# Optimization experiments

Hardware: AMD Instinct MI355X
Metric: run time of the kernel (lower is better)

## Reference

```python
import jax, jax.numpy as jnp
import numpy as np

B, S, W, E, H, V, C = 32, 512, 15, 300, 256, 50000, 2
G = 3 * H  # stacked GRU gate dim


def setup_inputs() -> dict:
    key = jax.random.key(0)
    ks = jax.random.split(key, 20)
    f = lambda k, shape, s=0.05: jax.random.normal(k, shape, dtype=jnp.float32) * s
    return {
        "x": jax.random.randint(ks[0], (B, S), 0, V),
        "x_pre": jax.random.randint(ks[1], (B, S), 0, V),
        "x_alt": jax.random.randint(ks[2], (B, S), 0, V),
        "x_cur": jax.random.randint(ks[3], (B, S), 0, V),
        "seq_lens": jax.random.randint(ks[4], (B,), 1, S),
        "emb": f(ks[5], (V, E), 0.1),
        "W_ih_f": f(ks[6], (G, E)), "W_hh_f": f(ks[7], (G, H)),
        "b_ih_f": jnp.zeros((G,), jnp.float32), "b_hh_f": jnp.zeros((G,), jnp.float32),
        "W_ih_b": f(ks[8], (G, E)), "W_hh_b": f(ks[9], (G, H)),
        "b_ih_b": jnp.zeros((G,), jnp.float32), "b_hh_b": jnp.zeros((G,), jnp.float32),
        "bn_gamma": jnp.ones((2 * H,), jnp.float32), "bn_beta": jnp.zeros((2 * H,), jnp.float32),
        "mlp_W": f(ks[10], (2 * H, 2 * H)), "mlp_b": jnp.zeros((2 * H,), jnp.float32),
        "lin_W": f(ks[11], (C, 2 * H)), "lin_b": jnp.zeros((C,), jnp.float32),
    }


def _gru_last(xs, Wih, Whh, bih, bhh, reverse):
    """xs: [T, N, E]; returns final hidden state [N, H] of a torch-style GRU."""
    xp = jnp.einsum('tne,ge->tng', xs, Wih) + bih  # precompute input projections
    h0 = jnp.zeros((xs.shape[1], Whh.shape[1]), xs.dtype)

    def step(h, xg):
        hg = h @ Whh.T + bhh
        xr, xz, xn = jnp.split(xg, 3, axis=-1)
        hr, hz, hn = jnp.split(hg, 3, axis=-1)
        r = jax.nn.sigmoid(xr + hr)
        z = jax.nn.sigmoid(xz + hz)
        n = jnp.tanh(xn + r * hn)
        return (1.0 - z) * n + z * h, None

    h, _ = jax.lax.scan(step, h0, xp, reverse=reverse)
    return h


def reference(x, x_pre, x_alt, x_cur, seq_lens, emb,
              W_ih_f, W_hh_f, b_ih_f, b_hh_f,
              W_ih_b, W_hh_b, b_ih_b, b_hh_b,
              bn_gamma, bn_beta, mlp_W, mlp_b, lin_W, lin_b):
    mask = (x > 0).astype(jnp.float32)[:, :, None]            # [B,S,1]
    idx = jnp.arange(S)[:, None] + jnp.arange(W)[None, :]      # [S,W] window gather
    # torch pads the id tensor with 0 then embeds -> pad rows embed to emb[0]
    ef = emb[jnp.pad(x, ((0, 0), (W - 1, 0)))]                 # [B,S+W-1,E]
    et = emb[jnp.pad(x, ((0, 0), (0, W - 1)))]
    fwin = ef[:, idx].transpose(2, 0, 1, 3).reshape(W, B * S, E)
    twin = et[:, idx].transpose(2, 0, 1, 3).reshape(W, B * S, E)
    hf = _gru_last(fwin, W_ih_f, W_hh_f, b_ih_f, b_hh_f, False).reshape(B, S, H)
    hb = _gru_last(twin, W_ih_b, W_hh_b, b_ih_b, b_hh_b, True).reshape(B, S, H)
    hidden = jnp.concatenate([hf * mask, hb * mask], axis=2)   # [B,S,2H]
    # BatchNorm1d (training-mode batch stats, per channel over B and S)
    mu = hidden.mean(axis=(0, 1))
    var = ((hidden - mu) ** 2).mean(axis=(0, 1))
    normed = ((hidden - mu) / jnp.sqrt(var + 1e-5)) * bn_gamma + bn_beta
    normed = normed * mask
    mlp_h = (normed @ mlp_W.T + mlp_b) * mask + (mask - 1.0) * 65500.0
    pooled = mlp_h.max(axis=1)                                 # [B,2H] masked max-pool
    return pooled @ lin_W.T + lin_b                            # [B,C]
```

## Files before the change

### kernel.cpp

```cpp
#include <hip/hip_runtime.h>
#include <hip/hip_bf16.h>
#include <stdint.h>


typedef unsigned short u16;
typedef unsigned int u32;
typedef float f32x16 __attribute__((ext_vector_type(16)));
typedef float f32x4  __attribute__((ext_vector_type(4)));
typedef short bf16x8 __attribute__((ext_vector_type(8)));

#define MFMA32 __builtin_amdgcn_mfma_f32_32x32x16_bf16
#define MFMA16 __builtin_amdgcn_mfma_f32_16x16x32_bf16

#define NB 32
#define NS 512
#define NW 15
#define NE 300
#define NH 256
#define NG 768
#define NCELL (NB*NS)
#define EPAD 320
#define MRE 32
#define MRR 64
#define HS 264
#define WROWS 78
#define RZS 260
#define NSS 264

__device__ __forceinline__ float bf2f(u16 u){
    union { unsigned int i; float f; } v; v.i = ((unsigned int)u) << 16; return v.f;
}
__device__ __forceinline__ u16 f2bf(float f){
    union { float f; unsigned int i; } v; v.f = f;
    unsigned int x = v.i;
    x += 0x7fffu + ((x >> 16) & 1u);
    return (u16)(x >> 16);
}
__device__ __forceinline__ u16 f2bf_rh(float f){
    return (u16)((__float_as_uint(f) + 0x8000u) >> 16);
}
__device__ __forceinline__ unsigned fkey(float f){
    unsigned b = __float_as_uint(f);
    return b ^ ((b & 0x80000000u) ? 0xFFFFFFFFu : 0x80000000u);
}

__device__ __forceinline__ float sigm_hw(float x){
    return __builtin_amdgcn_rcpf(1.0f + __builtin_amdgcn_exp2f(x * -1.44269504f));
}
__device__ __forceinline__ float tanh_hw(float x){
    return fmaf(-2.0f, __builtin_amdgcn_rcpf(1.0f + __builtin_amdgcn_exp2f(x * 2.88539008f)), 1.0f);
}

__global__ void prep_kernel(const float* __restrict__ Wih_f, const float* __restrict__ Wih_b,
                            const float* __restrict__ Whh_f, const float* __restrict__ Whh_b,
                            const float* __restrict__ mlpW,
                            u16* __restrict__ WihF_p, u16* __restrict__ WihB_p,
                            u16* __restrict__ WhhF_p, u16* __restrict__ WhhB_p,
                            u16* __restrict__ mlpW_p,
                            float* __restrict__ bnSum, float* __restrict__ bnSumSq,
                            unsigned* __restrict__ pooled_u)
{
    const int tid  = blockIdx.x*blockDim.x + threadIdx.x;
    const int nthr = gridDim.x*blockDim.x;
    for (int i = tid; i < 3*8*20*64; i += nthr){
        const int lane = i & 63;
        const int t2   = i >> 6;
        const int kc   = t2 % 20;
        const int wvg  = t2 / 20;
        const int g    = wvg >> 3, wv = wvg & 7;
        const int col  = wv*32 + (lane & 31);
        const int k0   = kc*16 + (lane >> 5)*8;
        const float* sF = Wih_f + (size_t)(g*NH + col)*NE;
        const float* sB = Wih_b + (size_t)(g*NH + col)*NE;
        u16* dF = WihF_p + (size_t)i*8;
        u16* dB = WihB_p + (size_t)i*8;
        #pragma unroll
        for (int j = 0; j < 8; j++){
            const int k = k0 + j;
            dF[j] = (k < NE) ? f2bf(sF[k]) : (u16)0;
            dB[j] = (k < NE) ? f2bf(sB[k]) : (u16)0;
        }
    }
    for (int i = tid; i < 3*16*8*64; i += nthr){
        const int lane = i & 63;
        const int kc   = (i >> 6) & 7;
        const int wvg  = i >> 9;
        const int g    = wvg >> 4, wv = wvg & 15;
        const int l15  = lane & 15, q = lane >> 4;
        const int col  = wv*16 + l15;
        const int k0   = kc*32 + q*8;
        const float* srcF = Whh_f + (size_t)(g*NH + col)*NH + k0;
        const float* srcB = Whh_b + (size_t)(g*NH + col)*NH + k0;
        u16* dF = WhhF_p + (size_t)i*8;
        u16* dB = WhhB_p + (size_t)i*8;
        #pragma unroll
        for (int j = 0; j < 8; j++){ dF[j] = f2bf(srcF[j]); dB[j] = f2bf(srcB[j]); }
    }
    for (int i = tid; i < 2*8*32*64; i += nthr){
        const int lane = i & 63;
        const int t2   = i >> 6;
        const int kc   = t2 & 31;
        const int ntwv = t2 >> 5;
        const int nt   = ntwv >> 3, wv = ntwv & 7;
        const int row  = wv*64 + nt*32 + (lane & 31);
        const int k0   = kc*16 + (lane >> 5)*8;
        const float* s = mlpW + (size_t)row*512 + k0;
        u16* d = mlpW_p + (size_t)i*8;
        #pragma unroll
        for (int j = 0; j < 8; j++) d[j] = f2bf(s[j]);
    }
    for (int i = tid; i < 512; i += nthr){ bnSum[i] = 0.0f; bnSumSq[i] = 0.0f; }
    for (int i = tid; i < NB*512; i += nthr) pooled_u[i] = 0u;
}

__global__ __launch_bounds__(512, 4)
void eproj_kernel(const int* __restrict__ x, const float* __restrict__ emb,
                  const u16* __restrict__ Wih_p, const float* __restrict__ b_ih,
                  const float* __restrict__ b_hh,
                  u32* __restrict__ xprojRZ, u16* __restrict__ xprojN)
{
    __shared__ u16 a_lds[MRE*328];
    const int tid = threadIdx.x;
    const int mb  = blockIdx.x;
    {
        const int row = tid >> 4, jj = tid & 15;
        const int flat = mb*MRE + row;
        const int t_id = (flat < NCELL) ? x[flat] : 0;
        const float4* src = (const float4*)(emb + (size_t)t_id*NE);
        u16* dst = a_lds + row*328;
        for (int idx = jj; idx < 75; idx += 16){
            float4 v = src[idx];
            ushort4 o; o.x=f2bf(v.x); o.y=f2bf(v.y); o.z=f2bf(v.z); o.w=f2bf(v.w);
            *(ushort4*)(dst + idx*4) = o;
        }
        if (jj == 15){
            const ushort4 z = {0,0,0,0};
            #pragma unroll
            for (int c = 300; c < 320; c += 4) *(ushort4*)(dst + c) = z;
        }
    }
    __syncthreads();

    const int lane = tid & 63, wv = tid >> 6, l31 = lane & 31, q = lane >> 5;
    const int col = wv*32 + l31;
    f32x16 acc[3];
    #pragma unroll
    for (int g = 0; g < 3; g++)
        #pragma unroll
        for (int i = 0; i < 16; i++) acc[g][i] = 0.0f;

    const u16* a0p = a_lds + l31*328 + q*8;
    const char* wf0 = (const char*)Wih_p + (size_t)((0*8 + wv)*20)*1024 + (size_t)lane*16;
    const char* wf1 = (const char*)Wih_p + (size_t)((1*8 + wv)*20)*1024 + (size_t)lane*16;
    const char* wf2 = (const char*)Wih_p + (size_t)((2*8 + wv)*20)*1024 + (size_t)lane*16;

    #pragma unroll 4
    for (int kc = 0; kc < 20; kc++){
        bf16x8 a0 = *(const bf16x8*)(a0p + kc*16);
        bf16x8 b0 = *(const bf16x8*)(wf0 + kc*1024);
        bf16x8 b1 = *(const bf16x8*)(wf1 + kc*1024);
        bf16x8 b2 = *(const bf16x8*)(wf2 + kc*1024);
        acc[0] = MFMA32(a0,b0,acc[0],0,0,0);
        acc[1] = MFMA32(a0,b1,acc[1],0,0,0);
        acc[2] = MFMA32(a0,b2,acc[2],0,0,0);
    }
    const float br  = b_ih[col]      + b_hh[col];
    const float bz  = b_ih[NH+col]   + b_hh[NH+col];
    const float bn_ = b_ih[2*NH+col];
    #pragma unroll
    for (int r = 0; r < 16; r++){
        const int rit = (r&3) + 8*(r>>2) + 4*q;
        const int row = mb*MRE + rit;
        const u32 rzv = (u32)f2bf(acc[0][r] + br) | ((u32)f2bf(acc[1][r] + bz) << 16);
        xprojRZ[(size_t)row*256 + col] = rzv;
        xprojN [(size_t)row*256 + col] = f2bf(acc[2][r] + bn_);
    }
}

__global__ __launch_bounds__(1024, 4)
void recur_kernel(const int* __restrict__ x,
                  const u32* __restrict__ xprojRZ, const u16* __restrict__ xprojN,
                  const u16* __restrict__ Whh_p, const float* __restrict__ b_hh,
                  u16* __restrict__ hidden, float* __restrict__ bnSum, float* __restrict__ bnSumSq,
                  int dir)
{
    __shared__ u32 rz_lds[WROWS*RZS];
    __shared__ u16 n_lds [WROWS*NSS];
    __shared__ u16 h_lds [MRR*HS];
    __shared__ float maskv[MRR];
    const int tid = threadIdx.x;
    const int bid = blockIdx.x;
    const int mb  = ((bid & 7) << 5) | (bid >> 3);
    if (tid < MRR) maskv[tid] = (x[mb*MRR + tid] > 0) ? 1.0f : 0.0f;

    const int bidx = (mb*MRR) >> 9;
    const int s0   = (mb*MRR) & (NS-1);
    const int joff = s0 + (dir ? 0 : -(NW-1));

    for (int i = tid; i < WROWS*64; i += 1024){
        const int w = i >> 6, c4 = i & 63;
        const int j = joff + w;
        const size_t row = ((unsigned)j < (unsigned)NS) ? (size_t)(bidx*NS + j) : (size_t)NCELL;
        const uint4 v = *(const uint4*)(xprojRZ + row*256 + c4*4);
        *(uint4*)(rz_lds + w*RZS + c4*4) = v;
    }
    for (int i = tid; i < WROWS*32; i += 1024){
        const int w = i >> 5, c8 = i & 31;
        const int j = joff + w;
        const size_t row = ((unsigned)j < (unsigned)NS) ? (size_t)(bidx*NS + j) : (size_t)NCELL;
        const uint4 v = *(const uint4*)(xprojN + row*256 + c8*8);
        *(uint4*)(n_lds + w*NSS + c8*8) = v;
    }
    __syncthreads();

    const int lane = tid & 63, wv = tid >> 6;
    const int l15 = lane & 15, q = lane >> 4;
    const int col  = wv*16 + l15;

    const float bhn = b_hh[2*NH + col];

    const char* wf = (const char*)Whh_p + ((size_t)wv << 13) + ((size_t)lane << 4);

    const int haOff = l15*HS + q*8;
    const u32* rzp0 = rz_lds + q*4*RZS + col;
    const u16* nnp0 = n_lds  + q*4*NSS + col;

    float hreg[16];
    #pragma unroll
    for (int i = 0; i < 16; i++) hreg[i] = 0.0f;

    #pragma unroll 1
    for (int t = 0; t < NW; t++){
        f32x4 acc[4][3];
        #pragma unroll
        for (int mt = 0; mt < 4; mt++)
            #pragma unroll
            for (int g = 0; g < 3; g++)
                #pragma unroll
                for (int i = 0; i < 4; i++) acc[mt][g][i] = (g == 2) ? bhn : 0.0f;

        if (t > 0){
            const u16* hcur = h_lds + haOff;
            bf16x8 b0 = *(const bf16x8*)(wf + 0*131072);
            bf16x8 b1 = *(const bf16x8*)(wf + 1*131072);
            bf16x8 b2 = *(const bf16x8*)(wf + 2*131072);
            #pragma unroll
            for (int kc = 0; kc < 8; kc++){
                bf16x8 n0, n1, n2;
                if (kc < 7){
                    const int ko = (kc+1)*1024;
                    n0 = *(const bf16x8*)(wf + 0*131072 + ko);
                    n1 = *(const bf16x8*)(wf + 1*131072 + ko);
                    n2 = *(const bf16x8*)(wf + 2*131072 + ko);
                }
                bf16x8 a0 = *(const bf16x8*)(hcur + kc*32 +   0);
                bf16x8 a1 = *(const bf16x8*)(hcur + kc*32 + 16*HS);
                bf16x8 a2 = *(const bf16x8*)(hcur + kc*32 + 32*HS);
                bf16x8 a3 = *(const bf16x8*)(hcur + kc*32 + 48*HS);
                acc[0][0] = MFMA16(a0,b0,acc[0][0],0,0,0);
                acc[1][0] = MFMA16(a1,b0,acc[1][0],0,0,0);
                acc[2][0] = MFMA16(a2,b0,acc[2][0],0,0,0);
                acc[3][0] = MFMA16(a3,b0,acc[3][0],0,0,0);
                acc[0][1] = MFMA16(a0,b1,acc[0][1],0,0,0);
                acc[1][1] = MFMA16(a1,b1,acc[1][1],0,0,0);
                acc[2][1] = MFMA16(a2,b1,acc[2][1],0,0,0);
                acc[3][1] = MFMA16(a3,b1,acc[3][1],0,0,0);
                acc[0][2] = MFMA16(a0,b2,acc[0][2],0,0,0);
                acc[1][2] = MFMA16(a1,b2,acc[1][2],0,0,0);
                acc[2][2] = MFMA16(a2,b2,acc[2][2],0,0,0);
                acc[3][2] = MFMA16(a3,b2,acc[3][2],0,0,0);
                if (kc < 7){ b0 = n0; b1 = n1; b2 = n2; }
            }
        }
        const int wbase = (dir == 0) ? t : ((NW-1) - t);
        const u32* rzp = rzp0 + wbase*RZS;
        const u16* nnp = nnp0 + wbase*NSS;
        #pragma unroll
        for (int half = 0; half < 2; half++){
            u32 rz[8]; u16 nn[8];
            #pragma unroll
            for (int i = 0; i < 8; i++){
                const int ii = half*8 + i;
                const int mt = ii >> 2, r = ii & 3;
                rz[i] = rzp[(mt*16 + r)*RZS];
                nn[i] = nnp[(mt*16 + r)*NSS];
            }
            #pragma unroll
            for (int i = 0; i < 8; i++){
                const int ii = half*8 + i;
                const int mt = ii >> 2, r = ii & 3;
                const float xr = bf2f((u16)(rz[i] & 0xFFFFu));
                const float xz = bf2f((u16)(rz[i] >> 16));
                const float xn = bf2f(nn[i]);
                const float rg = sigm_hw(xr + acc[mt][0][r]);
                const float zg = sigm_hw(xz + acc[mt][1][r]);
                const float ng = tanh_hw(fmaf(rg, acc[mt][2][r], xn));
                hreg[ii] = fmaf(zg, hreg[ii] - ng, ng);
            }
        }
        if (t + 1 < NW){
            __syncthreads();
            #pragma unroll
            for (int mt = 0; mt < 4; mt++)
                #pragma unroll
                for (int r = 0; r < 4; r++){
                    const int rit = mt*16 + q*4 + r;
                    h_lds[rit*HS + col] = f2bf_rh(hreg[mt*4 + r]);
                }
            __syncthreads();
        }
    }
    float sum = 0.0f, sumsq = 0.0f;
    #pragma unroll
    for (int mt = 0; mt < 4; mt++)
        #pragma unroll
        for (int r = 0; r < 4; r++){
            const int rit = mt*16 + q*4 + r;
            const float hm = hreg[mt*4 + r] * maskv[rit];
            hidden[(size_t)(mb*MRR + rit)*512 + dir*NH + col] = f2bf(hm);
            sum += hm; sumsq += hm*hm;
        }
    sum   += __shfl_xor(sum, 16);   sumsq += __shfl_xor(sumsq, 16);
    sum   += __shfl_xor(sum, 32);   sumsq += __shfl_xor(sumsq, 32);
    if (q == 0){
        atomicAdd(&bnSum[dir*NH + col], sum);
        atomicAdd(&bnSumSq[dir*NH + col], sumsq);
    }
}

__global__ void bnfin_kernel(const float* __restrict__ bnSum, const float* __restrict__ bnSumSq,
                             const float* __restrict__ gamma, const float* __restrict__ beta,
                             float* __restrict__ bnScale, float* __restrict__ bnShift)
{
    const int c = blockIdx.x*blockDim.x + threadIdx.x;
    if (c < 512){
        const float mu  = bnSum[c]   * (1.0f/16384.0f);
        const float var = bnSumSq[c] * (1.0f/16384.0f) - mu*mu;
        const float inv = rsqrtf(var + 1e-5f);
        const float sc  = gamma[c]*inv;
        bnScale[c] = sc;
        bnShift[c] = beta[c] - mu*sc;
    }
}

__global__ __launch_bounds__(512, 4)
void mlp_kernel(const int* __restrict__ x, const u16* __restrict__ hidden,
                const u16* __restrict__ mlpW_p, const float* __restrict__ bnScale,
                const float* __restrict__ bnShift, const float* __restrict__ mlp_b,
                unsigned* __restrict__ pooled_u)
{
    __shared__ u16 a_lds[MRE*520];
    __shared__ float maskv[MRE];
    const int tid = threadIdx.x;
    const int mb  = blockIdx.x;
    if (tid < MRE) maskv[tid] = (x[mb*MRE + tid] > 0) ? 1.0f : 0.0f;
    __syncthreads();
    {
        const int row = tid >> 4, jj = tid & 15;
        const float m = maskv[row];
        const u16* src = hidden + (size_t)(mb*MRE + row)*512;
        u16* dst = a_lds + row*520;
        for (int c4 = jj; c4 < 128; c4 += 16){
            ushort4 v = ((const ushort4*)src)[c4];
            const int c = c4*4;
            float4 sc = *(const float4*)(bnScale + c);
            float4 sh = *(const float4*)(bnShift + c);
            ushort4 o;
            o.x = f2bf((bf2f(v.x)*sc.x + sh.x)*m);
            o.y = f2bf((bf2f(v.y)*sc.y + sh.y)*m);
            o.z = f2bf((bf2f(v.z)*sc.z + sh.z)*m);
            o.w = f2bf((bf2f(v.w)*sc.w + sh.w)*m);
            *(ushort4*)(dst + c) = o;
        }
    }
    __syncthreads();

    const int lane = tid & 63, wv = tid >> 6, l31 = lane & 31, q = lane >> 5;
    f32x16 acc[2];
    #pragma unroll
    for (int g = 0; g < 2; g++)
        #pragma unroll
        for (int i = 0; i < 16; i++) acc[g][i] = 0.0f;

    const u16* a0p = a_lds + l31*520 + q*8;
    const char* wm0 = (const char*)mlpW_p + (size_t)((0*8 + wv)*32)*1024 + (size_t)lane*16;
    const char* wm1 = (const char*)mlpW_p + (size_t)((1*8 + wv)*32)*1024 + (size_t)lane*16;

    #pragma unroll 4
    for (int kc = 0; kc < 32; kc++){
        bf16x8 a0 = *(const bf16x8*)(a0p + kc*16);
        bf16x8 b0 = *(const bf16x8*)(wm0 + kc*1024);
        bf16x8 b1 = *(const bf16x8*)(wm1 + kc*1024);
        acc[0] = MFMA32(a0,b0,acc[0],0,0,0);
        acc[1] = MFMA32(a0,b1,acc[1],0,0,0);
    }

    const int bidx = mb >> 4;
    #pragma unroll
    for (int nt = 0; nt < 2; nt++){
        const int colg = wv*64 + nt*32 + l31;
        const float bias = mlp_b[colg];
        float mx = -3.4e38f;
        #pragma unroll
        for (int r = 0; r < 16; r++){
            const int rit = (r&3) + 8*(r>>2) + 4*q;
            const float m = maskv[rit];
            const float v = (acc[nt][r] + bias)*m + (m - 1.0f)*65500.0f;
            mx = fmaxf(mx, v);
        }
        mx = fmaxf(mx, __shfl_xor(mx, 32));
        if (q == 0) atomicMax(&pooled_u[bidx*512 + colg], fkey(mx));
    }
}

__global__ void final_kernel(const unsigned* __restrict__ pooled_u,
                             const float* __restrict__ linW, const float* __restrict__ linb,
                             float* __restrict__ out)
{
    const int b = blockIdx.x;
    const int lane = threadIdx.x;
    float s0 = 0.0f, s1 = 0.0f;
    for (int c = lane; c < 512; c += 64){
        const unsigned u = pooled_u[b*512 + c];
        const unsigned bits = (u & 0x80000000u) ? (u ^ 0x80000000u) : ~u;
        const float f = __uint_as_float(bits);
        s0 += f * linW[c];
        s1 += f * linW[512 + c];
    }
    #pragma unroll
    for (int off = 32; off > 0; off >>= 1){
        s0 += __shfl_xor(s0, off);
        s1 += __shfl_xor(s1, off);
    }
    if (lane == 0){ out[2*b] = s0 + linb[0]; out[2*b + 1] = s1 + linb[1]; }
}

extern "C" void kernel_launch(void* const* d_in, const int* in_sizes, int n_in,
                              void* d_out, int out_size, void* d_ws, size_t ws_size,
                              hipStream_t stream)
{
    const int*   x     = (const int*)  d_in[0];
    const float* emb   = (const float*)d_in[5];
    const float* Wih_f = (const float*)d_in[6];
    const float* Whh_f = (const float*)d_in[7];
    const float* bih_f = (const float*)d_in[8];
    const float* bhh_f = (const float*)d_in[9];
    const float* Wih_b = (const float*)d_in[10];
    const float* Whh_b = (const float*)d_in[11];
    const float* bih_b = (const float*)d_in[12];
    const float* bhh_b = (const float*)d_in[13];
    const float* gamma = (const float*)d_in[14];
    const float* beta  = (const float*)d_in[15];
    const float* mlpW  = (const float*)d_in[16];
    const float* mlpb  = (const float*)d_in[17];
    const float* linW  = (const float*)d_in[18];
    const float* linb  = (const float*)d_in[19];
    float* out = (float*)d_out;
    char* ws = (char*)d_ws;

    u16*   WihF_p  = (u16*)  (ws + 0);
    u16*   WihB_p  = (u16*)  (ws + 491520);
    u16*   WhhF_p  = (u16*)  (ws + 983040);
    u16*   WhhB_p  = (u16*)  (ws + 1376256);
    u16*   mlpW_p  = (u16*)  (ws + 1769472);
    float* bnSum   = (float*)(ws + 2293760);
    float* bnSumSq = (float*)(ws + 2295808);
    float* bnScale = (float*)(ws + 2297856);
    float* bnShift = (float*)(ws + 2299904);
    unsigned* pooled_u = (unsigned*)(ws + 2301952);
    u16*   hidden  = (u16*)  (ws + 2367488);
    u32*   xprojRZ = (u32*)  (ws + 19144704);
    u16*   xprojN  = (u16*)  (ws + 35987456);

    prep_kernel<<<512, 256, 0, stream>>>(Wih_f, Wih_b, Whh_f, Whh_b, mlpW,
                                         WihF_p, WihB_p, WhhF_p, WhhB_p, mlpW_p,
                                         bnSum, bnSumSq, pooled_u);
    eproj_kernel<<<514, 512, 0, stream>>>(x, emb, WihF_p, bih_f, bhh_f, xprojRZ, xprojN);
    recur_kernel<<<256, 1024, 0, stream>>>(x, xprojRZ, xprojN, WhhF_p, bhh_f, hidden, bnSum, bnSumSq, 0);
    eproj_kernel<<<514, 512, 0, stream>>>(x, emb, WihB_p, bih_b, bhh_b, xprojRZ, xprojN);
    recur_kernel<<<256, 1024, 0, stream>>>(x, xprojRZ, xprojN, WhhB_p, bhh_b, hidden, bnSum, bnSumSq, 1);

    bnfin_kernel<<<2, 256, 0, stream>>>(bnSum, bnSumSq, gamma, beta, bnScale, bnShift);
    mlp_kernel<<<512, 512, 0, stream>>>(x, hidden, mlpW_p, bnScale, bnShift, mlpb, pooled_u);
    final_kernel<<<32, 64, 0, stream>>>(pooled_u, linW, linb, out);
}
```

Before: 487.7 us.

## Double-buffer GRU hidden state in LDS and read n-gate projections from global

The recurrent kernel now keeps two hidden-state buffers in LDS and alternates between them each step. This removes one of the two barriers per timestep. It also stops staging the n-gate input projections into LDS and loads them straight from global memory at each step. Together this frees LDS and cuts prologue copy time, which could allow higher occupancy, at the cost of per-step scattered 2-byte global loads on the recurrence critical path.

```diff
diff --git a/kernel.cpp b/kernel.cpp
--- a/kernel.cpp
+++ b/kernel.cpp
@@ -25,7 +25,6 @@
 #define HS 264
 #define WROWS 78
 #define RZS 260
-#define NSS 264
 
 __device__ __forceinline__ float bf2f(u16 u){
     union { unsigned int i; float f; } v; v.i = ((unsigned int)u) << 16; return v.f;
@@ -185,8 +184,7 @@
                   int dir)
 {
     __shared__ u32 rz_lds[WROWS*RZS];
-    __shared__ u16 n_lds [WROWS*NSS];
-    __shared__ u16 h_lds [MRR*HS];
+    __shared__ u16 hb[2][MRR*HS];
     __shared__ float maskv[MRR];
     const int tid = threadIdx.x;
     const int bid = blockIdx.x;
@@ -204,13 +202,6 @@
         const uint4 v = *(const uint4*)(xprojRZ + row*256 + c4*4);
         *(uint4*)(rz_lds + w*RZS + c4*4) = v;
     }
-    for (int i = tid; i < WROWS*32; i += 1024){
-        const int w = i >> 5, c8 = i & 31;
-        const int j = joff + w;
-        const size_t row = ((unsigned)j < (unsigned)NS) ? (size_t)(bidx*NS + j) : (size_t)NCELL;
-        const uint4 v = *(const uint4*)(xprojN + row*256 + c8*8);
-        *(uint4*)(n_lds + w*NSS + c8*8) = v;
-    }
     __syncthreads();
 
     const int lane = tid & 63, wv = tid >> 6;
@@ -223,7 +214,10 @@
 
     const int haOff = l15*HS + q*8;
     const u32* rzp0 = rz_lds + q*4*RZS + col;
-    const u16* nnp0 = n_lds  + q*4*NSS + col;
+    const char* xnb = (const char*)xprojN;
+    const u32 colN  = (u32)(col * 2);
+    const u32 rowBaseN = (u32)(bidx * NS) * 512u;
+    const u32 padN  = (u32)NCELL * 512u + colN;
 
     float hreg[16];
     #pragma unroll
@@ -240,7 +234,7 @@
                 for (int i = 0; i < 4; i++) acc[mt][g][i] = (g == 2) ? bhn : 0.0f;
 
         if (t > 0){
-            const u16* hcur = h_lds + haOff;
+            const u16* hcur = hb[t & 1] + haOff;
             bf16x8 b0 = *(const bf16x8*)(wf + 0*131072);
             bf16x8 b1 = *(const bf16x8*)(wf + 1*131072);
             bf16x8 b2 = *(const bf16x8*)(wf + 2*131072);
@@ -273,17 +267,24 @@
             }
         }
         const int wbase = (dir == 0) ? t : ((NW-1) - t);
+        const int jbase = joff + wbase;
+        u16 nn[16];
+        #pragma unroll
+        for (int i = 0; i < 16; i++){
+            const int mt = i >> 2, r = i & 3;
+            const int j = jbase + mt*16 + q*4 + r;
+            const u32 off = ((unsigned)j < (unsigned)NS) ? (rowBaseN + (u32)j*512u + colN) : padN;
+            nn[i] = *(const u16*)(xnb + off);
+        }
         const u32* rzp = rzp0 + wbase*RZS;
-        const u16* nnp = nnp0 + wbase*NSS;
         #pragma unroll
         for (int half = 0; half < 2; half++){
-            u32 rz[8]; u16 nn[8];
+            u32 rz[8];
             #pragma unroll
             for (int i = 0; i < 8; i++){
                 const int ii = half*8 + i;
                 const int mt = ii >> 2, r = ii & 3;
                 rz[i] = rzp[(mt*16 + r)*RZS];
-                nn[i] = nnp[(mt*16 + r)*NSS];
             }
             #pragma unroll
             for (int i = 0; i < 8; i++){
@@ -291,7 +292,7 @@
                 const int mt = ii >> 2, r = ii & 3;
                 const float xr = bf2f((u16)(rz[i] & 0xFFFFu));
                 const float xz = bf2f((u16)(rz[i] >> 16));
-                const float xn = bf2f(nn[i]);
+                const float xn = bf2f(nn[ii]);
                 const float rg = sigm_hw(xr + acc[mt][0][r]);
                 const float zg = sigm_hw(xz + acc[mt][1][r]);
                 const float ng = tanh_hw(fmaf(rg, acc[mt][2][r], xn));
@@ -299,13 +300,13 @@
             }
         }
         if (t + 1 < NW){
-            __syncthreads();
+            u16* hw = hb[(t + 1) & 1];
             #pragma unroll
             for (int mt = 0; mt < 4; mt++)
                 #pragma unroll
                 for (int r = 0; r < 4; r++){
                     const int rit = mt*16 + q*4 + r;
-                    h_lds[rit*HS + col] = f2bf_rh(hreg[mt*4 + r]);
+                    hw[rit*HS + col] = f2bf_rh(hreg[mt*4 + r]);
                 }
             __syncthreads();
         }
```

Result: slower. 659.1 us (+35.2%).
